# Optimization experiments

Hardware: AMD Instinct MI355X
Metric: run time of the kernel (lower is better)

## Reference

```python
import jax, jax.numpy as jnp
import numpy as np

EPS = 1e-8  # torch cosine_similarity norm clamp


def _l2_normalize(x):
    # normalize last dim with torch-style eps clamp on the norm
    n = jnp.linalg.norm(x, axis=-1, keepdims=True)
    return x / jnp.maximum(n, EPS)


def setup_inputs() -> dict:
    key = jax.random.key(0)
    ks = jax.random.split(key, 6)
    T, Nq, D = 4, 4096, 1024
    Ns, H, P, C = 2048, 3, 256, 100
    return {
        "query_tube_feats": jax.random.normal(ks[0], (T, Nq, D), jnp.float32),
        "support_feats": jax.random.normal(ks[1], (Ns, D), jnp.float32),
        "head_W": jax.random.normal(ks[2], (H, D, P), jnp.float32) * (1.0 / np.sqrt(D)),
        "head_b": jax.random.normal(ks[3], (H, P), jnp.float32) * 0.01,
        "cls_W": jax.random.normal(ks[4], (D, C), jnp.float32) * (1.0 / np.sqrt(D)),
        "cls_b": jax.random.normal(ks[5], (C,), jnp.float32) * 0.01,
    }


def reference(query_tube_feats, support_feats, head_W, head_b, cls_W, cls_b):
    # aggregate_features with 'mean' aggregation over the tube/frame axis
    agg_query = jnp.mean(query_tube_feats, axis=0)                 # [Nq, D]

    # all 3 relation heads at once: Linear projections
    q = jnp.einsum('nd,hdp->hnp', agg_query, head_W) + head_b[:, None, :]   # [H, Nq, P]
    s = jnp.einsum('md,hdp->hmp', support_feats, head_W) + head_b[:, None, :]  # [H, Ns, P]

    # cosine similarity as fused normalize + GEMM (same math as broadcast cosine)
    qn = _l2_normalize(q)
    sn = _l2_normalize(s)
    dists = jnp.einsum('hnp,hmp->hnm', qn, sn)                     # [H, Nq, Ns]

    match_scores = jnp.mean(dists, axis=0)                         # [Nq, Ns]
    support_preds = support_feats @ cls_W + cls_b                  # [Ns, C]
    return match_scores, support_preds
```

## Files before the change

kernel.cpp:

```cpp
#include <hip/hip_runtime.h>

#define NQ 4096
#define NS 2048
#define DD 1024
#define HH 3
#define PP 256
#define CC 100

typedef __attribute__((ext_vector_type(8))) short bf16x8;
typedef __attribute__((ext_vector_type(4))) float f32x4;

#define AS1 __attribute__((address_space(1)))
#define AS3 __attribute__((address_space(3)))

__device__ __forceinline__ void gload16(const void* g, void* l) {
  __builtin_amdgcn_global_load_lds((const AS1 unsigned int*)g,
                                   (AS3 unsigned int*)l, 16, 0, 0);
}

__device__ __forceinline__ unsigned short f2bf(float f) {
  union { float f; unsigned u; } v; v.f = f;
  return (unsigned short)((v.u + 0x7FFFu + ((v.u >> 16) & 1u)) >> 16);
}

__global__ __launch_bounds__(256) void prep_kernel(
    const float* __restrict__ q,
    const float* __restrict__ sup,
    const float* __restrict__ hW,
    const float* __restrict__ cW,
    unsigned short* __restrict__ Xq,
    unsigned short* __restrict__ Xs,
    unsigned short* __restrict__ Wt,
    unsigned short* __restrict__ WcT)
{
  __shared__ unsigned short T[64][72];
  const int b = blockIdx.x, t = threadIdx.x;

  if (b < 1536) {
    if (b < 1024) {
      #pragma unroll
      for (int i = 0; i < 4; ++i) {
        int idx = (b * 1024 + i * 256 + t) * 4;
        const float4 a  = *(const float4*)&q[idx];
        const float4 c1 = *(const float4*)&q[NQ * DD + idx];
        const float4 c2 = *(const float4*)&q[2 * NQ * DD + idx];
        const float4 c3 = *(const float4*)&q[3 * NQ * DD + idx];
        ushort4 o;
        o.x = f2bf((a.x + c1.x + c2.x + c3.x) * 0.25f);
        o.y = f2bf((a.y + c1.y + c2.y + c3.y) * 0.25f);
        o.z = f2bf((a.z + c1.z + c2.z + c3.z) * 0.25f);
        o.w = f2bf((a.w + c1.w + c2.w + c3.w) * 0.25f);
        *(ushort4*)&Xq[idx] = o;
      }
    } else {
      #pragma unroll
      for (int i = 0; i < 4; ++i) {
        int idx = ((b - 1024) * 1024 + i * 256 + t) * 4;
        const float4 a = *(const float4*)&sup[idx];
        ushort4 o;
        o.x = f2bf(a.x); o.y = f2bf(a.y); o.z = f2bf(a.z); o.w = f2bf(a.w);
        *(ushort4*)&Xs[idx] = o;
      }
    }
    return;
  }

  const float* src; unsigned short* dst; int srcC, pvalid, k0, p0;
  if (b < 1728) {
    int r = b - 1536; int h = r / 64; int rr = r % 64;
    k0 = (rr >> 2) * 64; p0 = (rr & 3) * 64;
    src = hW + h * DD * PP; srcC = PP; pvalid = PP;
    dst = Wt + (h * PP + p0) * DD;
  } else {
    int r = b - 1728;
    k0 = (r >> 1) * 64; p0 = (r & 1) * 64;
    src = cW; srcC = CC; pvalid = CC;
    dst = WcT + p0 * DD;
  }
  {
    int kl = t >> 2, pb = (t & 3) * 4;
    #pragma unroll
    for (int j = 0; j < 4; ++j) {
      int pl = pb + j * 16;
      int p = p0 + pl;
      float4 v; v.x = v.y = v.z = v.w = 0.f;
      if (p + 3 < pvalid) {
        v = *(const float4*)&src[(k0 + kl) * srcC + p];
      } else {
        if (p + 0 < pvalid) v.x = src[(k0 + kl) * srcC + p + 0];
        if (p + 1 < pvalid) v.y = src[(k0 + kl) * srcC + p + 1];
        if (p + 2 < pvalid) v.z = src[(k0 + kl) * srcC + p + 2];
        if (p + 3 < pvalid) v.w = src[(k0 + kl) * srcC + p + 3];
      }
      T[kl][pl + 0] = f2bf(v.x); T[kl][pl + 1] = f2bf(v.y);
      T[kl][pl + 2] = f2bf(v.z); T[kl][pl + 3] = f2bf(v.w);
    }
    __syncthreads();
    int pr = t >> 2, kb = (t & 3) * 4;
    #pragma unroll
    for (int j = 0; j < 4; ++j) {
      int kk = kb + j * 16;
      ushort4 o;
      o.x = T[kk + 0][pr]; o.y = T[kk + 1][pr];
      o.z = T[kk + 2][pr]; o.w = T[kk + 3][pr];
      *(ushort4*)&dst[pr * DD + k0 + kk] = o;
    }
  }
}

__global__ __launch_bounds__(256) void proj_kernel(
    const unsigned short* __restrict__ Xq,
    const unsigned short* __restrict__ Xs,
    const unsigned short* __restrict__ Wt,
    const float* __restrict__ hb,
    unsigned short* __restrict__ Qn,
    unsigned short* __restrict__ Sn)
{
  __shared__ unsigned short As[2][64 * 64];
  __shared__ unsigned short Bs[2][256 * 64];

  const int bid0 = blockIdx.x;
  const int bid = (bid0 & 7) * 36 + (bid0 >> 3);
  const int h = bid / 96;
  const int r = bid % 96;
  const unsigned short* src; unsigned short* dst; int row0; float scale;
  if (r < 64) { src = Xq; dst = Qn; row0 = r * 64; scale = 1.f / 3.f; }
  else        { src = Xs; dst = Sn; row0 = (r - 64) * 64; scale = 1.f; }

  const int tid = threadIdx.x;
  const int w = tid >> 6, l = tid & 63;
  const int rA = l & 15, kg = l >> 4;
  const unsigned short* wbase = Wt + h * PP * DD;

  auto STAGE = [&](int buf, int kt) {
    #pragma unroll
    for (int i = 0; i < 10; ++i) {
      int c = w + i * 4;
      if (c < 8)
        gload16(src + (row0 + c * 8 + (l >> 3)) * DD + kt * 64 + (l & 7) * 8,
                &As[buf][c * 512]);
      else
        gload16(wbase + ((c - 8) * 8 + (l >> 3)) * DD + kt * 64 + (l & 7) * 8,
                &Bs[buf][(c - 8) * 512]);
    }
  };

  f32x4 acc[4][4] = {};
  STAGE(0, 0);
  __syncthreads();
  int cur = 0;
  for (int kt = 0; kt < DD / 64; ++kt) {
    if (kt + 1 < DD / 64) STAGE(cur ^ 1, kt + 1);
    #pragma unroll
    for (int kk = 0; kk < 2; ++kk) {
      bf16x8 a[4], bfr[4];
      #pragma unroll
      for (int mi = 0; mi < 4; ++mi)
        a[mi] = *(const bf16x8*)&As[cur][(mi * 16 + rA) * 64 + kk * 32 + kg * 8];
      #pragma unroll
      for (int ni = 0; ni < 4; ++ni)
        bfr[ni] = *(const bf16x8*)&Bs[cur][(w * 64 + ni * 16 + rA) * 64 + kk * 32 + kg * 8];
      #pragma unroll
      for (int mi = 0; mi < 4; ++mi)
        #pragma unroll
        for (int ni = 0; ni < 4; ++ni)
          acc[mi][ni] =
              __builtin_amdgcn_mfma_f32_16x16x32_bf16(a[mi], bfr[ni], acc[mi][ni], 0, 0, 0);
    }
    __syncthreads();
    cur ^= 1;
  }

  float* rowsq = (float*)&As[0][0];
  unsigned short* Ct = (unsigned short*)&Bs[0][0];
  float bias[4];
  #pragma unroll
  for (int ni = 0; ni < 4; ++ni)
    bias[ni] = hb[h * PP + w * 64 + ni * 16 + rA];

  #pragma unroll
  for (int mi = 0; mi < 4; ++mi) {
    #pragma unroll
    for (int i = 0; i < 4; ++i) {
      float s = 0.f;
      #pragma unroll
      for (int ni = 0; ni < 4; ++ni) {
        float v = acc[mi][ni][i] + bias[ni];
        acc[mi][ni][i] = v;
        s += v * v;
      }
      s += __shfl_xor(s, 1);
      s += __shfl_xor(s, 2);
      s += __shfl_xor(s, 4);
      s += __shfl_xor(s, 8);
      if (rA == 0) rowsq[w * 64 + mi * 16 + kg * 4 + i] = s;
    }
  }
  __syncthreads();
  #pragma unroll
  for (int mi = 0; mi < 4; ++mi) {
    #pragma unroll
    for (int i = 0; i < 4; ++i) {
      int row = mi * 16 + kg * 4 + i;
      float tot = rowsq[row] + rowsq[64 + row] + rowsq[128 + row] + rowsq[192 + row];
      float inv = scale / fmaxf(sqrtf(tot), 1e-8f);
      #pragma unroll
      for (int ni = 0; ni < 4; ++ni)
        Ct[row * 264 + w * 64 + ni * 16 + rA] = f2bf(acc[mi][ni][i] * inv);
    }
  }
  __syncthreads();
  #pragma unroll
  for (int pass = 0; pass < 16; ++pass) {
    int row = pass * 4 + (tid >> 6);
    int c = tid & 63;
    ushort4 o = *(const ushort4*)&Ct[row * 264 + c * 4];
    *(ushort4*)&dst[(row0 + row) * (HH * PP) + h * PP + c * 4] = o;
  }
}

__global__ __launch_bounds__(256) void mm_kernel(
    const unsigned short* __restrict__ Qn,
    const unsigned short* __restrict__ Sn,
    const unsigned short* __restrict__ Xs,
    const unsigned short* __restrict__ WcT,
    const float* __restrict__ cb,
    float* __restrict__ out)
{
  __shared__ __align__(16) char smem[128 * 132 * 4];
  unsigned short* As = (unsigned short*)smem;
  unsigned short* Bs = (unsigned short*)(smem + 32768);
  float* Ct = (float*)smem;

  const int bid = blockIdx.x;
  const int tid = threadIdx.x;
  const int w = tid >> 6, l = tid & 63;
  const int wm = w >> 1, wn = w & 1;
  const int rA = l & 15, kg = l >> 4;

  const unsigned short *A, *B;
  int ldk, nkt, bm, bn;
  const bool match = bid < 512;
  if (match) {
    int xcd = bid & 7, idx = bid >> 3;
    bm = xcd * 4 + (idx & 3);
    bn = idx >> 2;
    A = Qn + bm * 128 * (HH * PP);
    B = Sn + bn * 128 * (HH * PP);
    ldk = HH * PP; nkt = (HH * PP) / 64;
  } else {
    bm = bid - 512; bn = 0;
    A = Xs + bm * 128 * DD;
    B = WcT;
    ldk = DD; nkt = DD / 64;
  }

  auto STAGE = [&](int buf, int kt) {
    #pragma unroll
    for (int i = 0; i < 8; ++i) {
      int c = w + i * 4;
      if (c < 16)
        gload16(A + (c * 8 + (l >> 3)) * ldk + kt * 64 + (l & 7) * 8,
                &As[buf * 8192 + c * 512]);
      else
        gload16(B + ((c - 16) * 8 + (l >> 3)) * ldk + kt * 64 + (l & 7) * 8,
                &Bs[buf * 8192 + (c - 16) * 512]);
    }
  };

  f32x4 acc[4][4] = {};
  STAGE(0, 0);
  __syncthreads();
  int cur = 0;
  for (int kt = 0; kt < nkt; ++kt) {
    if (kt + 1 < nkt) STAGE(cur ^ 1, kt + 1);
    #pragma unroll
    for (int kk = 0; kk < 2; ++kk) {
      bf16x8 a[4], bfr[4];
      #pragma unroll
      for (int mi = 0; mi < 4; ++mi)
        a[mi] = *(const bf16x8*)&As[cur * 8192 + (wm * 64 + mi * 16 + rA) * 64 + kk * 32 + kg * 8];
      #pragma unroll
      for (int ni = 0; ni < 4; ++ni)
        bfr[ni] = *(const bf16x8*)&Bs[cur * 8192 + (wn * 64 + ni * 16 + rA) * 64 + kk * 32 + kg * 8];
      #pragma unroll
      for (int mi = 0; mi < 4; ++mi)
        #pragma unroll
        for (int ni = 0; ni < 4; ++ni)
          acc[mi][ni] =
              __builtin_amdgcn_mfma_f32_16x16x32_bf16(a[mi], bfr[ni], acc[mi][ni], 0, 0, 0);
    }
    __syncthreads();
    cur ^= 1;
  }

  if (match) {
    #pragma unroll
    for (int mi = 0; mi < 4; ++mi)
      #pragma unroll
      for (int i = 0; i < 4; ++i) {
        int row = wm * 64 + mi * 16 + kg * 4 + i;
        #pragma unroll
        for (int ni = 0; ni < 4; ++ni)
          Ct[row * 132 + wn * 64 + ni * 16 + rA] = acc[mi][ni][i];
      }
    __syncthreads();
    #pragma unroll
    for (int pass = 0; pass < 16; ++pass) {
      int row = pass * 8 + (tid >> 5);
      int c = tid & 31;
      f32x4 v = *(const f32x4*)&Ct[row * 132 + c * 4];
      *(f32x4*)&out[(long)(bm * 128 + row) * NS + bn * 128 + c * 4] = v;
    }
  } else {
    float* o2 = out + (long)NQ * NS;
    #pragma unroll
    for (int mi = 0; mi < 4; ++mi)
      #pragma unroll
      for (int i = 0; i < 4; ++i) {
        int row = bm * 128 + wm * 64 + mi * 16 + kg * 4 + i;
        #pragma unroll
        for (int ni = 0; ni < 4; ++ni) {
          int col = wn * 64 + ni * 16 + rA;
          if (col < CC) o2[row * CC + col] = acc[mi][ni][i] + cb[col];
        }
      }
  }
}

extern "C" void kernel_launch(void* const* d_in, const int* in_sizes, int n_in,
                              void* d_out, int out_size, void* d_ws, size_t ws_size,
                              hipStream_t stream) {
  const float* q   = (const float*)d_in[0];
  const float* sup = (const float*)d_in[1];
  const float* hW  = (const float*)d_in[2];
  const float* hb  = (const float*)d_in[3];
  const float* cW  = (const float*)d_in[4];
  const float* cb  = (const float*)d_in[5];
  float* out = (float*)d_out;

  char* ws = (char*)d_ws;
  unsigned short* Xq  = (unsigned short*)(ws + 0);
  unsigned short* Xs  = (unsigned short*)(ws + (8u  << 20));
  unsigned short* Wt  = (unsigned short*)(ws + (12u << 20));
  unsigned short* WcT = (unsigned short*)(ws + (12u << 20) + 1572864u);
  unsigned short* Qn  = (unsigned short*)(ws + (14u << 20));
  unsigned short* Sn  = (unsigned short*)(ws + (20u << 20));

  prep_kernel<<<1760, 256, 0, stream>>>(q, sup, hW, cW, Xq, Xs, Wt, WcT);
  proj_kernel<<<288, 256, 0, stream>>>(Xq, Xs, Wt, hb, Qn, Sn);
  mm_kernel<<<512 + 16, 256, 0, stream>>>(Qn, Sn, Xs, WcT, cb, out);
}
```

Measured before the change: 183.7 us.

## Retile projection GEMM to square 128x128 tiles and split normalization into separate kernel

The projection GEMM now treats Xq and Xs as one concatenated 6144-row matrix (relying on their adjacent workspace placement) multiplied against all three heads' weights. It uses 128x128 tiles with a 2x2 wave layout instead of 64x256 per-head tiles, which gives more balanced A/B reuse per block. The per-row L2 normalization moves out of the GEMM epilogue into a new lightweight kernel that rereads the bf16 output, normalizes each head with wave shuffles, and writes it back in place. The cost is an extra launch, an extra read/write pass over QS, and normalization computed from bf16-rounded values instead of fp32.

```diff
diff --git a/kernel.cpp b/kernel.cpp
--- a/kernel.cpp
+++ b/kernel.cpp
@@ -6,6 +6,8 @@
 #define HH 3
 #define PP 256
 #define CC 100
+#define NR (NQ + NS)
+#define PN (HH * PP)
 
 typedef __attribute__((ext_vector_type(8))) short bf16x8;
 typedef __attribute__((ext_vector_type(4))) float f32x4;
@@ -21,6 +23,11 @@
 __device__ __forceinline__ unsigned short f2bf(float f) {
   union { float f; unsigned u; } v; v.f = f;
   return (unsigned short)((v.u + 0x7FFFu + ((v.u >> 16) & 1u)) >> 16);
+}
+
+__device__ __forceinline__ float bf2f(unsigned short s) {
+  union { unsigned u; float f; } v; v.u = ((unsigned)s) << 16;
+  return v.f;
 }
 
 __global__ __launch_bounds__(256) void prep_kernel(
@@ -108,40 +115,38 @@
   }
 }
 
-__global__ __launch_bounds__(256) void proj_kernel(
-    const unsigned short* __restrict__ Xq,
-    const unsigned short* __restrict__ Xs,
-    const unsigned short* __restrict__ Wt,
-    const float* __restrict__ hb,
-    unsigned short* __restrict__ Qn,
-    unsigned short* __restrict__ Sn)
+__global__ __launch_bounds__(256) void pgemm_kernel(
+    const unsigned short* __restrict__ X,
+    const unsigned short* __restrict__ Wall,
+    const float* __restrict__ ball,
+    unsigned short* __restrict__ QS)
 {
-  __shared__ unsigned short As[2][64 * 64];
-  __shared__ unsigned short Bs[2][256 * 64];
-
-  const int bid0 = blockIdx.x;
-  const int bid = (bid0 & 7) * 36 + (bid0 >> 3);
-  const int h = bid / 96;
-  const int r = bid % 96;
-  const unsigned short* src; unsigned short* dst; int row0; float scale;
-  if (r < 64) { src = Xq; dst = Qn; row0 = r * 64; scale = 1.f / 3.f; }
-  else        { src = Xs; dst = Sn; row0 = (r - 64) * 64; scale = 1.f; }
-
+  __shared__ __align__(16) char smem[65536];
+  unsigned short* As = (unsigned short*)smem;
+  unsigned short* Bs = (unsigned short*)(smem + 32768);
+  unsigned short* Ct = (unsigned short*)smem;
+
+  const int bid = blockIdx.x;
+  const int swz = (bid & 7) * 36 + (bid >> 3);
+  const int bm = swz / 6, bn = swz % 6;
   const int tid = threadIdx.x;
   const int w = tid >> 6, l = tid & 63;
+  const int wm = w >> 1, wn = w & 1;
   const int rA = l & 15, kg = l >> 4;
-  const unsigned short* wbase = Wt + h * PP * DD;
+
+  const unsigned short* A = X + bm * 128 * DD;
+  const unsigned short* B = Wall + bn * 128 * DD;
 
   auto STAGE = [&](int buf, int kt) {
     #pragma unroll
-    for (int i = 0; i < 10; ++i) {
+    for (int i = 0; i < 8; ++i) {
       int c = w + i * 4;
-      if (c < 8)
-        gload16(src + (row0 + c * 8 + (l >> 3)) * DD + kt * 64 + (l & 7) * 8,
-                &As[buf][c * 512]);
+      if (c < 16)
+        gload16(A + (c * 8 + (l >> 3)) * DD + kt * 64 + (l & 7) * 8,
+                &As[buf * 8192 + c * 512]);
       else
-        gload16(wbase + ((c - 8) * 8 + (l >> 3)) * DD + kt * 64 + (l & 7) * 8,
-                &Bs[buf][(c - 8) * 512]);
+        gload16(B + ((c - 16) * 8 + (l >> 3)) * DD + kt * 64 + (l & 7) * 8,
+                &Bs[buf * 8192 + (c - 16) * 512]);
     }
   };
 
@@ -156,10 +161,10 @@
       bf16x8 a[4], bfr[4];
       #pragma unroll
       for (int mi = 0; mi < 4; ++mi)
-        a[mi] = *(const bf16x8*)&As[cur][(mi * 16 + rA) * 64 + kk * 32 + kg * 8];
+        a[mi] = *(const bf16x8*)&As[cur * 8192 + (wm * 64 + mi * 16 + rA) * 64 + kk * 32 + kg * 8];
       #pragma unroll
       for (int ni = 0; ni < 4; ++ni)
-        bfr[ni] = *(const bf16x8*)&Bs[cur][(w * 64 + ni * 16 + rA) * 64 + kk * 32 + kg * 8];
+        bfr[ni] = *(const bf16x8*)&Bs[cur * 8192 + (wn * 64 + ni * 16 + rA) * 64 + kk * 32 + kg * 8];
       #pragma unroll
       for (int mi = 0; mi < 4; ++mi)
         #pragma unroll
@@ -171,51 +176,60 @@
     cur ^= 1;
   }
 
-  float* rowsq = (float*)&As[0][0];
-  unsigned short* Ct = (unsigned short*)&Bs[0][0];
   float bias[4];
   #pragma unroll
   for (int ni = 0; ni < 4; ++ni)
-    bias[ni] = hb[h * PP + w * 64 + ni * 16 + rA];
-
-  #pragma unroll
-  for (int mi = 0; mi < 4; ++mi) {
+    bias[ni] = ball[bn * 128 + wn * 64 + ni * 16 + rA];
+
+  #pragma unroll
+  for (int mi = 0; mi < 4; ++mi)
     #pragma unroll
     for (int i = 0; i < 4; ++i) {
-      float s = 0.f;
-      #pragma unroll
-      for (int ni = 0; ni < 4; ++ni) {
-        float v = acc[mi][ni][i] + bias[ni];
-        acc[mi][ni][i] = v;
-        s += v * v;
-      }
-      s += __shfl_xor(s, 1);
-      s += __shfl_xor(s, 2);
-      s += __shfl_xor(s, 4);
-      s += __shfl_xor(s, 8);
-      if (rA == 0) rowsq[w * 64 + mi * 16 + kg * 4 + i] = s;
-    }
-  }
+      int row = wm * 64 + mi * 16 + kg * 4 + i;
+      #pragma unroll
+      for (int ni = 0; ni < 4; ++ni)
+        Ct[row * 136 + wn * 64 + ni * 16 + rA] = f2bf(acc[mi][ni][i] + bias[ni]);
+    }
   __syncthreads();
   #pragma unroll
-  for (int mi = 0; mi < 4; ++mi) {
-    #pragma unroll
-    for (int i = 0; i < 4; ++i) {
-      int row = mi * 16 + kg * 4 + i;
-      float tot = rowsq[row] + rowsq[64 + row] + rowsq[128 + row] + rowsq[192 + row];
-      float inv = scale / fmaxf(sqrtf(tot), 1e-8f);
-      #pragma unroll
-      for (int ni = 0; ni < 4; ++ni)
-        Ct[row * 264 + w * 64 + ni * 16 + rA] = f2bf(acc[mi][ni][i] * inv);
-    }
-  }
-  __syncthreads();
-  #pragma unroll
   for (int pass = 0; pass < 16; ++pass) {
-    int row = pass * 4 + (tid >> 6);
-    int c = tid & 63;
-    ushort4 o = *(const ushort4*)&Ct[row * 264 + c * 4];
-    *(ushort4*)&dst[(row0 + row) * (HH * PP) + h * PP + c * 4] = o;
+    int row = pass * 8 + (tid >> 5);
+    int c = tid & 31;
+    ushort4 v = *(const ushort4*)&Ct[row * 136 + c * 4];
+    *(ushort4*)&QS[(bm * 128 + row) * PN + bn * 128 + c * 4] = v;
+  }
+}
+
+__global__ __launch_bounds__(256) void norm_kernel(
+    unsigned short* __restrict__ QS)
+{
+  const int wid = blockIdx.x * 4 + (threadIdx.x >> 6);
+  const int l = threadIdx.x & 63;
+  unsigned short* rowp = QS + wid * PN;
+  const float scale = (wid < NQ) ? (1.f / 3.f) : 1.f;
+
+  float v[3][4];
+  float ss[3];
+  #pragma unroll
+  for (int h = 0; h < 3; ++h) {
+    ushort4 u = *(const ushort4*)&rowp[h * PP + l * 4];
+    v[h][0] = bf2f(u.x); v[h][1] = bf2f(u.y);
+    v[h][2] = bf2f(u.z); v[h][3] = bf2f(u.w);
+    ss[h] = v[h][0]*v[h][0] + v[h][1]*v[h][1] + v[h][2]*v[h][2] + v[h][3]*v[h][3];
+  }
+  #pragma unroll
+  for (int s = 1; s < 64; s <<= 1) {
+    ss[0] += __shfl_xor(ss[0], s);
+    ss[1] += __shfl_xor(ss[1], s);
+    ss[2] += __shfl_xor(ss[2], s);
+  }
+  #pragma unroll
+  for (int h = 0; h < 3; ++h) {
+    float inv = scale / fmaxf(sqrtf(ss[h]), 1e-8f);
+    ushort4 o;
+    o.x = f2bf(v[h][0] * inv); o.y = f2bf(v[h][1] * inv);
+    o.z = f2bf(v[h][2] * inv); o.w = f2bf(v[h][3] * inv);
+    *(ushort4*)&rowp[h * PP + l * 4] = o;
   }
 }
 
@@ -245,9 +259,9 @@
     int xcd = bid & 7, idx = bid >> 3;
     bm = xcd * 4 + (idx & 3);
     bn = idx >> 2;
-    A = Qn + bm * 128 * (HH * PP);
-    B = Sn + bn * 128 * (HH * PP);
-    ldk = HH * PP; nkt = (HH * PP) / 64;
+    A = Qn + bm * 128 * PN;
+    B = Sn + bn * 128 * PN;
+    ldk = PN; nkt = PN / 64;
   } else {
     bm = bid - 512; bn = 0;
     A = Xs + bm * 128 * DD;
@@ -344,10 +358,12 @@
   unsigned short* Xs  = (unsigned short*)(ws + (8u  << 20));
   unsigned short* Wt  = (unsigned short*)(ws + (12u << 20));
   unsigned short* WcT = (unsigned short*)(ws + (12u << 20) + 1572864u);
-  unsigned short* Qn  = (unsigned short*)(ws + (14u << 20));
-  unsigned short* Sn  = (unsigned short*)(ws + (20u << 20));
+  unsigned short* QS  = (unsigned short*)(ws + (14u << 20));
+  unsigned short* Qn  = QS;
+  unsigned short* Sn  = QS + (size_t)NQ * PN;
 
   prep_kernel<<<1760, 256, 0, stream>>>(q, sup, hW, cW, Xq, Xs, Wt, WcT);
-  proj_kernel<<<288, 256, 0, stream>>>(Xq, Xs, Wt, hb, Qn, Sn);
+  pgemm_kernel<<<288, 256, 0, stream>>>(Xq, Wt, hb, QS);
+  norm_kernel<<<NR / 4, 256, 0, stream>>>(QS);
   mm_kernel<<<512 + 16, 256, 0, stream>>>(Qn, Sn, Xs, WcT, cb, out);
 }
```

Result: no change. 181.7 us (-1.1%).
